# Kernel tuning notes

Measured on AMD Instinct MI355X. Metric: run time of the kernel, lower is better.

## Reference

```python
import jax, jax.numpy as jnp
import numpy as np

NUM_EMB = 256
EMB_DIM = 128
COMMIT_COST = 0.25


def setup_inputs() -> dict:
    key = jax.random.key(0)
    k1, k2 = jax.random.split(key)
    z = jax.random.normal(k1, (64, EMB_DIM, 64, 64), dtype=jnp.float32)
    # codebook initialized uniform(-1/num_embeddings, 1/num_embeddings)
    emb = jax.random.uniform(k2, (NUM_EMB, EMB_DIM), dtype=jnp.float32,
                             minval=-1.0 / NUM_EMB, maxval=1.0 / NUM_EMB)
    return {"z": z, "emb": emb}


def reference(z, emb):
    B, C, H, W = z.shape
    # [B, C, H, W] -> [B*H*W, C]
    z_flat = jnp.transpose(z, (0, 2, 3, 1)).reshape(-1, C)
    # squared L2 distances to each code: ||z||^2 - 2 z.e + ||e||^2, shape [N, K]
    d = (jnp.sum(z_flat * z_flat, axis=1, keepdims=True)
         - 2.0 * jnp.einsum('nc,kc->nk', z_flat, emb)
         + jnp.sum(emb * emb, axis=1))
    idx = jnp.argmin(d, axis=1)  # [N]
    # gather codes, back to NCHW
    quantized = emb[idx].reshape(B, H, W, C)
    quantized = jnp.transpose(quantized, (0, 3, 1, 2))
    commitment_loss = COMMIT_COST * jnp.mean(
        (jax.lax.stop_gradient(quantized) - z) ** 2)
    codebook_loss = jnp.mean((quantized - jax.lax.stop_gradient(z)) ** 2)
    # straight-through estimator
    quantized_ste = z + jax.lax.stop_gradient(quantized - z)
    return (quantized_ste, idx.reshape(B, H, W), commitment_loss, codebook_loss)
```

## Files before the change

### kernel.cpp

```cpp
#include <hip/hip_runtime.h>

#define K_EMB   256
#define C_DIM   128
#define HW      4096
#define NPOS    262144
#define Q_ELEMS 33554432
#define IDX_OFF Q_ELEMS
#define LOSS_OFF (Q_ELEMS + NPOS)

#define BLKP 64
#define TK   64
#define NQ   4

#define WS_ENORM 0
#define WS_ACC   256
#define WS_EMBT  512
#define WS_NEED_FULL  ((WS_EMBT + C_DIM * K_EMB) * 4)

__global__ __launch_bounds__(K_EMB) void vq_transpose(const float* __restrict__ emb,
                                                      float* __restrict__ ws,
                                                      int use_embT) {
    const int c = blockIdx.x, k = threadIdx.x;
    if (use_embT) ws[WS_EMBT + c * K_EMB + k] = emb[k * C_DIM + c];
    if (c == 0 && k == 0) ws[WS_ACC] = 0.f;
}

__global__ __launch_bounds__(K_EMB) void vq_enorm(const float* __restrict__ emb,
                                                  float* __restrict__ ws) {
    const int k = threadIdx.x;
    const float4* __restrict__ er = reinterpret_cast<const float4*>(emb + k * C_DIM);
    float s = 0.f;
    #pragma unroll
    for (int j = 0; j < C_DIM / 4; ++j) {
        float4 v = er[j];
        s = fmaf(v.x, v.x, s);
        s = fmaf(v.y, v.y, s);
        s = fmaf(v.z, v.z, s);
        s = fmaf(v.w, v.w, s);
    }
    ws[WS_ENORM + k] = s;
}

template <int UT>
__global__ __launch_bounds__(256, 4) void vq_main(const float* __restrict__ z,
                                                  const float* __restrict__ emb,
                                                  const float* __restrict__ ws,
                                                  float* __restrict__ out,
                                                  float* __restrict__ loss_acc) {
    __shared__ float zlds[C_DIM * BLKP];
    __shared__ float sh_best[256];
    __shared__ int   sh_bidx[256];

    const int t   = threadIdx.x;
    const int p   = t & (BLKP - 1);
    const int kq  = t >> 6;
    const int blk = blockIdx.x;
    const int b   = blk >> 6;
    const int hw0 = (blk & 63) * BLKP;
    const size_t zoff = (size_t)b * (C_DIM * HW) + hw0;
    const float* __restrict__ zsrc = z + zoff;

    {
        const float4* __restrict__ zs4 = reinterpret_cast<const float4*>(zsrc);
        float4* __restrict__ zl4 = reinterpret_cast<float4*>(zlds);
        #pragma unroll
        for (int j = 0; j < (C_DIM * BLKP / 4) / 256; ++j) {
            const int i4 = t + j * 256;
            const int c  = i4 >> 4;
            const int p4 = i4 & 15;
            zl4[i4] = zs4[(size_t)c * (HW / 4) + p4];
        }
    }
    __syncthreads();

    const float* __restrict__ embT  = ws + WS_EMBT;
    const float* __restrict__ enorm = ws + WS_ENORM;

    const int kbase = __builtin_amdgcn_readfirstlane(kq * TK);

    float acc[TK];
    #pragma unroll
    for (int j = 0; j < TK; ++j) acc[j] = 0.f;
    float znorm = 0.f;

    #pragma unroll 2
    for (int c = 0; c < C_DIM; ++c) {
        const float zc = zlds[c * BLKP + p];
        znorm = fmaf(zc, zc, znorm);
        if (UT) {
            const float* __restrict__ ep = embT + c * K_EMB + kbase;
            #pragma unroll
            for (int j = 0; j < TK; ++j)
                acc[j] = fmaf(zc, ep[j], acc[j]);
        } else {
            #pragma unroll
            for (int j = 0; j < TK; ++j)
                acc[j] = fmaf(zc, emb[(kbase + j) * C_DIM + c], acc[j]);
        }
    }

    float best = 3.402823466e38f;
    int   bidx = 0;
    #pragma unroll
    for (int j = 0; j < TK; ++j) {
        const float d = (znorm - 2.0f * acc[j]) + enorm[kbase + j];
        if (d < best) { best = d; bidx = kbase + j; }
    }

    sh_best[t] = best;
    sh_bidx[t] = bidx;
    __syncthreads();

    if (kq == 0) {
        float bb = sh_best[p];
        int   bi = sh_bidx[p];
        #pragma unroll
        for (int q = 1; q < NQ; ++q) {
            const float bq = sh_best[q * BLKP + p];
            const int   iq = sh_bidx[q * BLKP + p];
            if (bq < bb) { bb = bq; bi = iq; }
        }
        const int fin = bi;
        const int pos = blk * BLKP + p;
        __builtin_nontemporal_store((float)fin, &out[IDX_OFF + pos]);

        float lsum = 0.f;
        float* qp = out + zoff + p;
        const float4* __restrict__ er =
            reinterpret_cast<const float4*>(emb + fin * C_DIM);
        #pragma unroll 4
        for (int j = 0; j < C_DIM / 4; ++j) {
            const float4 ev = er[j];
            const int c0 = j * 4;
            const float z0 = zlds[(c0 + 0) * BLKP + p];
            const float z1 = zlds[(c0 + 1) * BLKP + p];
            const float z2 = zlds[(c0 + 2) * BLKP + p];
            const float z3 = zlds[(c0 + 3) * BLKP + p];
            const float d0 = ev.x - z0, d1 = ev.y - z1;
            const float d2 = ev.z - z2, d3 = ev.w - z3;
            lsum = fmaf(d0, d0, lsum);
            lsum = fmaf(d1, d1, lsum);
            lsum = fmaf(d2, d2, lsum);
            lsum = fmaf(d3, d3, lsum);
            __builtin_nontemporal_store(z0 + d0, &qp[(size_t)(c0 + 0) * HW]);
            __builtin_nontemporal_store(z1 + d1, &qp[(size_t)(c0 + 1) * HW]);
            __builtin_nontemporal_store(z2 + d2, &qp[(size_t)(c0 + 2) * HW]);
            __builtin_nontemporal_store(z3 + d3, &qp[(size_t)(c0 + 3) * HW]);
        }

        #pragma unroll
        for (int off = 32; off > 0; off >>= 1)
            lsum += __shfl_down(lsum, off, 64);
        if (p == 0) atomicAdd(loss_acc, lsum);
    }
}

__global__ void vq_finalize(const float* __restrict__ loss_acc,
                            float* __restrict__ out_losses) {
    float S = loss_acc[0];
    float mean = S / (float)Q_ELEMS;
    out_losses[0] = 0.25f * mean;
    out_losses[1] = mean;
}

extern "C" void kernel_launch(void* const* d_in, const int* in_sizes, int n_in,
                              void* d_out, int out_size, void* d_ws, size_t ws_size,
                              hipStream_t stream) {
    const float* z   = (const float*)d_in[0];
    const float* emb = (const float*)d_in[1];
    float* out = (float*)d_out;
    float* ws  = (float*)d_ws;

    int use_embT = (ws_size >= (size_t)WS_NEED_FULL) ? 1 : 0;

    vq_transpose<<<C_DIM, K_EMB, 0, stream>>>(emb, ws, use_embT);
    vq_enorm<<<1, K_EMB, 0, stream>>>(emb, ws);
    if (use_embT)
        vq_main<1><<<NPOS / BLKP, 256, 0, stream>>>(z, emb, ws, out, ws + WS_ACC);
    else
        vq_main<0><<<NPOS / BLKP, 256, 0, stream>>>(z, emb, ws, out, ws + WS_ACC);
    vq_finalize<<<1, 1, 0, stream>>>(ws + WS_ACC, out + LOSS_OFF);
}
```

Baseline: 400.4 us.

## Process two positions per thread to reuse codebook loads across 128-position blocks

Doubles the block tile from 64 to 128 spatial positions so each thread accumulates distances for two positions, reusing every codebook value it loads for two FMAs. This halves the codebook load traffic per FMA in the distance loop. In exchange, register use doubles (two 64-entry accumulator arrays), LDS per block grows to 64KB, and occupancy drops to 2 blocks per CU. The epilogue still uses only the first 128 threads (two wavefronts) for the gather and store.

```diff
diff --git a/kernel.cpp b/kernel.cpp
--- a/kernel.cpp
+++ b/kernel.cpp
@@ -8,9 +8,10 @@
 #define IDX_OFF Q_ELEMS
 #define LOSS_OFF (Q_ELEMS + NPOS)
 
-#define BLKP 64
+#define BLKP 128
 #define TK   64
 #define NQ   4
+#define PP   2
 
 #define WS_ENORM 0
 #define WS_ACC   256
@@ -42,21 +43,21 @@
 }
 
 template <int UT>
-__global__ __launch_bounds__(256, 4) void vq_main(const float* __restrict__ z,
+__global__ __launch_bounds__(256, 2) void vq_main(const float* __restrict__ z,
                                                   const float* __restrict__ emb,
                                                   const float* __restrict__ ws,
                                                   float* __restrict__ out,
                                                   float* __restrict__ loss_acc) {
     __shared__ float zlds[C_DIM * BLKP];
-    __shared__ float sh_best[256];
-    __shared__ int   sh_bidx[256];
+    __shared__ float sh_best[NQ * BLKP];
+    __shared__ int   sh_bidx[NQ * BLKP];
 
-    const int t   = threadIdx.x;
-    const int p   = t & (BLKP - 1);
-    const int kq  = t >> 6;
-    const int blk = blockIdx.x;
-    const int b   = blk >> 6;
-    const int hw0 = (blk & 63) * BLKP;
+    const int t    = threadIdx.x;
+    const int lane = t & 63;
+    const int kq   = t >> 6;
+    const int blk  = blockIdx.x;
+    const int b    = blk >> 5;
+    const int hw0  = (blk & 31) * BLKP;
     const size_t zoff = (size_t)b * (C_DIM * HW) + hw0;
     const float* __restrict__ zsrc = z + zoff;
 
@@ -66,8 +67,8 @@
         #pragma unroll
         for (int j = 0; j < (C_DIM * BLKP / 4) / 256; ++j) {
             const int i4 = t + j * 256;
-            const int c  = i4 >> 4;
-            const int p4 = i4 & 15;
+            const int c  = i4 >> 5;
+            const int p4 = i4 & 31;
             zl4[i4] = zs4[(size_t)c * (HW / 4) + p4];
         }
     }
@@ -78,40 +79,54 @@
 
     const int kbase = __builtin_amdgcn_readfirstlane(kq * TK);
 
-    float acc[TK];
+    float acc0[TK], acc1[TK];
     #pragma unroll
-    for (int j = 0; j < TK; ++j) acc[j] = 0.f;
-    float znorm = 0.f;
+    for (int j = 0; j < TK; ++j) { acc0[j] = 0.f; acc1[j] = 0.f; }
+    float znorm0 = 0.f, znorm1 = 0.f;
 
     #pragma unroll 2
     for (int c = 0; c < C_DIM; ++c) {
-        const float zc = zlds[c * BLKP + p];
-        znorm = fmaf(zc, zc, znorm);
+        const float z0 = zlds[c * BLKP + lane];
+        const float z1 = zlds[c * BLKP + lane + 64];
+        znorm0 = fmaf(z0, z0, znorm0);
+        znorm1 = fmaf(z1, z1, znorm1);
         if (UT) {
             const float* __restrict__ ep = embT + c * K_EMB + kbase;
             #pragma unroll
-            for (int j = 0; j < TK; ++j)
-                acc[j] = fmaf(zc, ep[j], acc[j]);
+            for (int j = 0; j < TK; ++j) {
+                const float e = ep[j];
+                acc0[j] = fmaf(z0, e, acc0[j]);
+                acc1[j] = fmaf(z1, e, acc1[j]);
+            }
         } else {
             #pragma unroll
-            for (int j = 0; j < TK; ++j)
-                acc[j] = fmaf(zc, emb[(kbase + j) * C_DIM + c], acc[j]);
+            for (int j = 0; j < TK; ++j) {
+                const float e = emb[(kbase + j) * C_DIM + c];
+                acc0[j] = fmaf(z0, e, acc0[j]);
+                acc1[j] = fmaf(z1, e, acc1[j]);
+            }
         }
     }
 
-    float best = 3.402823466e38f;
-    int   bidx = 0;
+    float best0 = 3.402823466e38f, best1 = 3.402823466e38f;
+    int   bidx0 = 0, bidx1 = 0;
     #pragma unroll
     for (int j = 0; j < TK; ++j) {
-        const float d = (znorm - 2.0f * acc[j]) + enorm[kbase + j];
-        if (d < best) { best = d; bidx = kbase + j; }
+        const float en = enorm[kbase + j];
+        const float d0 = (znorm0 - 2.0f * acc0[j]) + en;
+        const float d1 = (znorm1 - 2.0f * acc1[j]) + en;
+        if (d0 < best0) { best0 = d0; bidx0 = kbase + j; }
+        if (d1 < best1) { best1 = d1; bidx1 = kbase + j; }
     }
 
-    sh_best[t] = best;
-    sh_bidx[t] = bidx;
+    sh_best[kq * BLKP + lane]      = best0;
+    sh_bidx[kq * BLKP + lane]      = bidx0;
+    sh_best[kq * BLKP + lane + 64] = best1;
+    sh_bidx[kq * BLKP + lane + 64] = bidx1;
     __syncthreads();
 
-    if (kq == 0) {
+    if (t < BLKP) {
+        const int p = t;
         float bb = sh_best[p];
         int   bi = sh_bidx[p];
         #pragma unroll
@@ -151,7 +166,7 @@
         #pragma unroll
         for (int off = 32; off > 0; off >>= 1)
             lsum += __shfl_down(lsum, off, 64);
-        if (p == 0) atomicAdd(loss_acc, lsum);
+        if (lane == 0) atomicAdd(loss_acc, lsum);
     }
 }
 
```

Result: slower. 600.5 us (+50.0%).
